# Kernel optimization log

Hardware: AMD Instinct MI355X
Metric: run time of the kernel (lower is better)

Reference implementation:

```python
import jax, jax.numpy as jnp
import numpy as np

BN_EPS = 1e-5
W_THRESH = 1e-4

def _conv(x, w, b):
    # 1x1 Conv1d == per-point linear: x [B,C,N], w [O,C], b [O]
    return jnp.einsum('oc,bcn->bon', w, x) + b[None, :, None]

def _bn(x, g, b):
    # BatchNorm1d in training mode: batch stats over (B, N) per channel
    m = x.mean(axis=(0, 2), keepdims=True)
    v = x.var(axis=(0, 2), keepdims=True)
    return g[None, :, None] * (x - m) * jax.lax.rsqrt(v + BN_EPS) + b[None, :, None]

def setup_inputs() -> dict:
    key = jax.random.key(0)
    ks = jax.random.split(key, 12)
    B, N = 32, 2048
    d = {}
    d['points'] = jax.random.normal(ks[0], (B, 3, N), dtype=jnp.float32)
    def W(k, o, i):
        return jax.random.normal(k, (o, i), dtype=jnp.float32) * 0.02
    # encoder
    d['e_w1'] = W(ks[1], 64, 3);      d['e_b1'] = jnp.zeros(64)
    d['e_g1'] = jnp.ones(64);         d['e_be1'] = jnp.zeros(64)
    d['e_w2'] = W(ks[2], 128, 64);    d['e_b2'] = jnp.zeros(128)
    d['e_g2'] = jnp.ones(128);        d['e_be2'] = jnp.zeros(128)
    d['e_w3'] = W(ks[3], 1024, 128);  d['e_b3'] = jnp.zeros(1024)
    d['e_g3'] = jnp.ones(1024);       d['e_be3'] = jnp.zeros(1024)
    # head
    d['h_w1'] = W(ks[4], 512, 1088);  d['h_b1'] = jnp.zeros(512)
    d['h_g1'] = jnp.ones(512);        d['h_be1'] = jnp.zeros(512)
    d['h_w2'] = W(ks[5], 256, 512);   d['h_b2'] = jnp.zeros(256)
    d['h_g2'] = jnp.ones(256);        d['h_be2'] = jnp.zeros(256)
    d['h_w3'] = W(ks[6], 128, 256);   d['h_b3'] = jnp.zeros(128)
    d['h_g3'] = jnp.ones(128);        d['h_be3'] = jnp.zeros(128)
    d['h_w4'] = W(ks[7], 1, 128);     d['h_b4'] = jnp.zeros(1)
    return d

def _forward(points, e_w1, e_b1, e_g1, e_be1, e_w2, e_b2, e_g2, e_be2,
             e_w3, e_b3, e_g3, e_be3, h_w1, h_b1, h_g1, h_be1,
             h_w2, h_b2, h_g2, h_be2, h_w3, h_b3, h_g3, h_be3, h_w4, h_b4):
    B, _, N = points.shape
    # PointNetEncoder
    x = jax.nn.relu(_bn(_conv(points, e_w1, e_b1), e_g1, e_be1))
    pointfeat = x                                  # [B,64,N]
    x = jax.nn.relu(_bn(_conv(x, e_w2, e_b2), e_g2, e_be2))
    x = _bn(_conv(x, e_w3, e_b3), e_g3, e_be3)      # [B,1024,N]
    g = jnp.max(x, axis=2, keepdims=True)           # [B,1024,1]
    feat = jnp.concatenate([jnp.broadcast_to(g, (B, 1024, N)), pointfeat], axis=1)  # [B,1088,N]
    # head
    y = jax.nn.relu(_bn(_conv(feat, h_w1, h_b1), h_g1, h_be1))
    y = jax.nn.relu(_bn(_conv(y, h_w2, h_b2), h_g2, h_be2))
    y = jax.nn.relu(_bn(_conv(y, h_w3, h_b3), h_g3, h_be3))
    y = _conv(y, h_w4, h_b4)                        # [B,1,N]
    weights = 1.0 + y[:, 0, :]                      # [B,N]
    # WLSFIT, fully batched. Index-selection in the torch loop is equivalent to
    # zeroing invalid weights; the <=3-valid fallback uses uniform weights.
    valid = weights > W_THRESH                      # [B,N] (constant wrt grads)
    nv = jnp.sum(valid, axis=1)                     # [B]
    w_eff = jnp.where((nv > 3)[:, None],
                      weights * valid.astype(weights.dtype),
                      jnp.ones_like(weights))
    A = jnp.concatenate([jnp.swapaxes(points[:, :2, :], 1, 2),
                         jnp.ones((B, N, 1), dtype=points.dtype)], axis=-1)  # [B,N,3]
    z = points[:, 2, :]                             # [B,N]
    XtWX = jnp.einsum('bni,bn,bnj->bij', A, w_eff, A)   # [B,3,3]
    XtY = jnp.einsum('bni,bn->bi', A, w_eff * z)         # [B,3]
    L = jnp.linalg.cholesky(XtWX)
    u = jax.scipy.linalg.solve_triangular(L, XtY[..., None], lower=True)
    beta = jax.scipy.linalg.solve_triangular(jnp.swapaxes(L, -1, -2), u, lower=False)[..., 0]
    return beta, weights

def reference(points, e_w1, e_b1, e_g1, e_be1, e_w2, e_b2, e_g2, e_be2,
              e_w3, e_b3, e_g3, e_be3, h_w1, h_b1, h_g1, h_be1,
              h_w2, h_b2, h_g2, h_be2, h_w3, h_b3, h_g3, h_be3, h_w4, h_b4):
    return _forward(points, e_w1, e_b1, e_g1, e_be1, e_w2, e_b2, e_g2, e_be2,
                    e_w3, e_b3, e_g3, e_be3, h_w1, h_b1, h_g1, h_be1,
                    h_w2, h_b2, h_g2, h_be2, h_w3, h_b3, h_g3, h_be3, h_w4, h_b4)
```

## Files before the change

kernel.cpp:

```cpp
#include <hip/hip_runtime.h>
#include <math.h>


#define M_TOTAL 65536
#define BN_EPS 1e-5f
#define W_THRESH 1e-4f

typedef __attribute__((ext_vector_type(8))) _Float16 f16x8;
typedef __attribute__((ext_vector_type(2))) _Float16 half2v;
typedef __attribute__((ext_vector_type(4))) float f32x4;

__device__ __forceinline__ unsigned short f2h(float f) {
    _Float16 h = (_Float16)f;
    return __builtin_bit_cast(unsigned short, h);
}
__device__ __forceinline__ float h2f(unsigned short u) {
    return (float)__builtin_bit_cast(_Float16, u);
}

__device__ __forceinline__ void cp16(unsigned short* lds, const unsigned short* g) {
    __builtin_amdgcn_global_load_lds(
        (const __attribute__((address_space(1))) unsigned int*)(const void*)g,
        (__attribute__((address_space(3))) unsigned int*)(void*)lds,
        16, 0, 0);
}

__global__ void k_wprep(const float* __restrict__ e_w2, const float* __restrict__ e_w3,
                        const float* __restrict__ hw1, const float* __restrict__ h_w2,
                        const float* __restrict__ h_w3,
                        unsigned short* We2, unsigned short* We3, unsigned short* Wh1,
                        unsigned short* Wh2, unsigned short* Wh3) {
    int t = blockIdx.x;
    const float* W; int ldw, KB; unsigned short* D; int rel;
    if (t < 16)       { W = e_w2;       ldw = 64;   KB = 2;  D = We2; rel = t; }
    else if (t < 272) { W = e_w3;       ldw = 128;  KB = 4;  D = We3; rel = t - 16; }
    else if (t < 336) { W = hw1 + 1024; ldw = 1088; KB = 2;  D = Wh1; rel = t - 272; }
    else if (t < 592) { W = h_w2;       ldw = 512;  KB = 16; D = Wh2; rel = t - 336; }
    else              { W = h_w3;       ldw = 256;  KB = 8;  D = Wh3; rel = t - 592; }
    int ot = rel & 7, kb = (rel >> 3) % KB, ob = rel / (8 * KB);
    int l = threadIdx.x;
    int o = ob * 128 + ot * 16 + (l & 15);
    int k = kb * 32 + (l >> 4) * 8;
    const float* src = W + (size_t)o * ldw + k;
    float4 wa = *(const float4*)src;
    float4 wb = *(const float4*)(src + 4);
    uint4 pk;
    pk.x = (unsigned)f2h(wa.x) | ((unsigned)f2h(wa.y) << 16);
    pk.y = (unsigned)f2h(wa.z) | ((unsigned)f2h(wa.w) << 16);
    pk.z = (unsigned)f2h(wb.x) | ((unsigned)f2h(wb.y) << 16);
    pk.w = (unsigned)f2h(wb.z) | ((unsigned)f2h(wb.w) << 16);
    *(uint4*)(D + (size_t)rel * 512 + l * 8) = pk;
}

__global__ void k_moments(const float* __restrict__ pts, float* __restrict__ momP) {
    float s[9] = {0,0,0,0,0,0,0,0,0};
    for (int m = blockIdx.x * 256 + threadIdx.x; m < M_TOTAL; m += gridDim.x * 256) {
        int b = m >> 11, n = m & 2047;
        const float* p = pts + b * 6144 + n;
        float x = p[0], y = p[2048], z = p[4096];
        s[0] += x; s[1] += y; s[2] += z;
        s[3] += x * x; s[4] += y * y; s[5] += z * z;
        s[6] += x * y; s[7] += x * z; s[8] += y * z;
    }
    for (int off = 32; off; off >>= 1)
#pragma unroll
        for (int i = 0; i < 9; i++) s[i] += __shfl_down(s[i], off);
    __shared__ float red[4][9];
    int lane = threadIdx.x & 63, wv = threadIdx.x >> 6;
    if (lane == 0)
        for (int i = 0; i < 9; i++) red[wv][i] = s[i];
    __syncthreads();
    if (threadIdx.x < 9)
        momP[blockIdx.x * 9 + threadIdx.x] =
            red[0][threadIdx.x] + red[1][threadIdx.x] + red[2][threadIdx.x] + red[3][threadIdx.x];
}

__global__ void k_e1fin(const float* __restrict__ momP, const float* __restrict__ w,
                        const float* __restrict__ bias, const float* __restrict__ g,
                        const float* __restrict__ be, float* __restrict__ a, float* __restrict__ s) {
    __shared__ float m9[9];
    if (threadIdx.x < 9) {
        float t = 0.f;
        for (int k = 0; k < 64; k++) t += momP[k * 9 + threadIdx.x];
        m9[threadIdx.x] = t;
    }
    __syncthreads();
    int o = threadIdx.x;
    float w0 = w[o * 3], w1 = w[o * 3 + 1], w2 = w[o * 3 + 2], b = bias[o];
    float wS1 = w0 * m9[0] + w1 * m9[1] + w2 * m9[2];
    float sum = wS1 + 65536.f * b;
    float sumsq = w0 * w0 * m9[3] + w1 * w1 * m9[4] + w2 * w2 * m9[5]
                + 2.f * (w0 * w1 * m9[6] + w0 * w2 * m9[7] + w1 * w2 * m9[8])
                + 2.f * b * wS1 + 65536.f * b * b;
    float mean = sum * (1.f / 65536.f);
    float var = sumsq * (1.f / 65536.f) - mean * mean;
    float ac = g[o] * rsqrtf(var + BN_EPS);
    a[o] = ac;
    s[o] = be[o] - mean * ac;
}

__global__ void k_e1(const float* __restrict__ pts, const float* __restrict__ w,
                     const float* __restrict__ bias, const float* __restrict__ av,
                     const float* __restrict__ sv, unsigned short* __restrict__ Y) {
    __shared__ float wl[192], bl[64], al[64], sl[64];
    int tid = threadIdx.x;
    if (tid < 192) wl[tid] = w[tid];
    if (tid < 64) { bl[tid] = bias[tid]; al[tid] = av[tid]; sl[tid] = sv[tid]; }
    __syncthreads();
    int m = blockIdx.x * 256 + tid;
    int b = m >> 11, n = m & 2047;
    const float* p = pts + b * 6144 + n;
    float px = p[0], py = p[2048], pz = p[4096];
    unsigned short* yr = Y + (size_t)m * 64;
#pragma unroll
    for (int o8 = 0; o8 < 64; o8 += 8) {
        unsigned pkw[4];
#pragma unroll
        for (int t = 0; t < 4; t++) {
            int o = o8 + t * 2;
            float v0 = fmaf(wl[o * 3 + 0], px, fmaf(wl[o * 3 + 1], py, fmaf(wl[o * 3 + 2], pz, bl[o])));
            float v1 = fmaf(wl[o * 3 + 3], px, fmaf(wl[o * 3 + 4], py, fmaf(wl[o * 3 + 5], pz, bl[o + 1])));
            float y0 = fmaxf(fmaf(al[o], v0, sl[o]), 0.f);
            float y1 = fmaxf(fmaf(al[o + 1], v1, sl[o + 1]), 0.f);
            pkw[t] = (unsigned)f2h(y0) | ((unsigned)f2h(y1) << 16);
        }
        uint4 pk; pk.x = pkw[0]; pk.y = pkw[1]; pk.z = pkw[2]; pk.w = pkw[3];
        *(uint4*)(yr + o8) = pk;
    }
}

__global__ void k_redfin(const float* __restrict__ Ps, const float* __restrict__ Pq,
                         int C, int S,
                         const float* __restrict__ g, const float* __restrict__ be,
                         float* __restrict__ a, float* __restrict__ s) {
    int cl = threadIdx.x & 63, strip = threadIdx.x >> 6;
    int c = blockIdx.x * 64 + cl;
    float sm = 0.f, q = 0.f;
    for (int k = strip; k < S; k += 16) {
        sm += Ps[(size_t)k * C + c];
        q += Pq[(size_t)k * C + c];
    }
    __shared__ float rs[16][64], rq[16][64];
    rs[strip][cl] = sm; rq[strip][cl] = q;
    __syncthreads();
    if (threadIdx.x < 64) {
        float S2 = 0.f, Q = 0.f;
#pragma unroll
        for (int t = 0; t < 16; t++) { S2 += rs[t][cl]; Q += rq[t][cl]; }
        float mean = S2 * (1.f / M_TOTAL);
        float var = Q * (1.f / M_TOTAL) - mean * mean;
        float ac = g[c] * rsqrtf(var + BN_EPS);
        a[c] = ac;
        s[c] = be[c] - mean * ac;
    }
}

template <bool STORE, bool MINMAX, bool BIAS_BO, bool BNB, int KB32, int CHUNKS, bool AREG>
__launch_bounds__(256, 2)
__global__ void k_mgemm(const unsigned short* __restrict__ Wf, int O,
                        const unsigned short* __restrict__ X,
                        const float* __restrict__ a_in, const float* __restrict__ s_in,
                        const float* __restrict__ bias,
                        unsigned short* __restrict__ Y,
                        float* __restrict__ Psum, float* __restrict__ Psq,
                        float* __restrict__ Pmax, float* __restrict__ Pmn) {
    constexpr int K = KB32 * 32;
    __shared__ __align__(16) unsigned short sB[2][4096];
    __shared__ __align__(16) unsigned short sA[AREG ? 2 : 2 * 4096];
    __shared__ __align__(16) short sT[STORE ? 64 * 136 : 2];
    __shared__ _Float16 sah[BNB ? K : 2], ssb[BNB ? K : 2];
    int tid = threadIdx.x;
    int lane = tid & 63, wave = tid >> 6;
    int wo = wave >> 1, wm = wave & 1;
    int m0 = blockIdx.x * (128 * CHUNKS), o0 = blockIdx.y * 128;
    int bidx = m0 >> 11;

    if constexpr (BNB)
        for (int c = tid; c < K; c += 256) {
            sah[c] = (_Float16)a_in[c];
            ssb[c] = (_Float16)s_in[c];
        }

    f16x8 aAll[AREG ? KB32 : 1][4];
    const unsigned short* aBase = Wf + (size_t)blockIdx.y * KB32 * 8 * 512 + lane * 8;
    if constexpr (AREG) {
#pragma unroll
        for (int kb = 0; kb < KB32; kb++)
#pragma unroll
            for (int i = 0; i < 4; i++)
                aAll[kb][i] = *(const f16x8*)(aBase + (size_t)(kb * 8 + wo * 4 + i) * 512);
    }

    f32x4 acc[4][4];
#pragma unroll
    for (int i = 0; i < 4; i++)
#pragma unroll
        for (int j = 0; j < 4; j++) acc[i][j] = (f32x4){0.f, 0.f, 0.f, 0.f};

    float sAcc[4][4] = {}, qAcc[4][4] = {};
    float mxA[4][4], mnA[4][4];
    if constexpr (MINMAX) {
#pragma unroll
        for (int i = 0; i < 4; i++)
#pragma unroll
            for (int r = 0; r < 4; r++) { mxA[i][r] = -3.4e38f; mnA[i][r] = 3.4e38f; }
    }

    auto stageB = [&](int c, int kb_, int buf) {
        const unsigned short* src =
            X + (size_t)(m0 + c * 128 + wave * 32 + (lane & 15)) * K + kb_ * 32 + ((lane >> 4) * 8);
        cp16(&sB[buf][(wave * 2) * 512], src);
        cp16(&sB[buf][(wave * 2 + 1) * 512], src + 16 * K);
    };
    auto stageA = [&](int kb_, int buf) {
        const unsigned short* src = aBase + (size_t)(kb_ * 8 + wave * 2) * 512;
        cp16(&sA[buf * 4096 + (wave * 2) * 512], src);
        cp16(&sA[buf * 4096 + (wave * 2 + 1) * 512], src + 512);
    };

    stageB(0, 0, 0);
    if constexpr (!AREG) stageA(0, 0);

    for (int c = 0; c < CHUNKS; c++) {
#pragma unroll
        for (int kb = 0; kb < KB32; kb++) {
            __syncthreads();
            bool last = (c == CHUNKS - 1) && (kb == KB32 - 1);
            if (!last) {
                int kn = (kb + 1) & (KB32 - 1);
                int cn = (kb == KB32 - 1) ? c + 1 : c;
                int nbuf = (kb + 1) & 1;
                stageB(cn, kn, nbuf);
                if constexpr (!AREG) stageA(kn, nbuf);
            }
            const int cur = kb & 1;
            f16x8 bf[4];
#pragma unroll
            for (int j = 0; j < 4; j++)
                bf[j] = *(const f16x8*)&sB[cur][((wm * 4 + j) * 64 + lane) * 8];

            if constexpr (BNB) {
                int ka = kb * 32 + (lane >> 4) * 8;
                half2v a2[4], s2[4];
#pragma unroll
                for (int t = 0; t < 4; t++) {
                    a2[t] = *(const half2v*)&sah[ka + 2 * t];
                    s2[t] = *(const half2v*)&ssb[ka + 2 * t];
                }
                half2v z2 = (half2v)(_Float16)0;
#pragma unroll
                for (int j = 0; j < 4; j++) {
                    half2v* p = (half2v*)&bf[j];
#pragma unroll
                    for (int t = 0; t < 4; t++)
                        p[t] = __builtin_elementwise_max(a2[t] * p[t] + s2[t], z2);
                }
            }

            if constexpr (AREG) {
#pragma unroll
                for (int i = 0; i < 4; i++)
#pragma unroll
                    for (int j = 0; j < 4; j++)
                        acc[i][j] = __builtin_amdgcn_mfma_f32_16x16x32_f16(aAll[kb][i], bf[j], acc[i][j], 0, 0, 0);
            } else {
                f16x8 af[4];
#pragma unroll
                for (int i = 0; i < 4; i++)
                    af[i] = *(const f16x8*)&sA[cur * 4096 + ((wo * 4 + i) * 64 + lane) * 8];
#pragma unroll
                for (int i = 0; i < 4; i++)
#pragma unroll
                    for (int j = 0; j < 4; j++)
                        acc[i][j] = __builtin_amdgcn_mfma_f32_16x16x32_f16(af[i], bf[j], acc[i][j], 0, 0, 0);
            }
        }

        int q = lane >> 4, lc = lane & 15;
#pragma unroll
        for (int i = 0; i < 4; i++)
#pragma unroll
            for (int j = 0; j < 4; j++)
#pragma unroll
                for (int r = 0; r < 4; r++) {
                    float v = acc[i][j][r];
                    sAcc[i][r] += v;
                    qAcc[i][r] = fmaf(v, v, qAcc[i][r]);
                    if constexpr (MINMAX) {
                        mxA[i][r] = fmaxf(mxA[i][r], v);
                        mnA[i][r] = fminf(mnA[i][r], v);
                    }
                }

        if constexpr (STORE) {
            int mbase = m0 + c * 128;
#pragma unroll
            for (int ch = 0; ch < 2; ch++) {
                if (wm == ch) {
#pragma unroll
                    for (int i = 0; i < 4; i++) {
                        int ob = o0 + wo * 64 + i * 16 + q * 4;
                        float b0 = BIAS_BO ? bias[bidx * O + ob + 0] : bias[ob + 0];
                        float b1 = BIAS_BO ? bias[bidx * O + ob + 1] : bias[ob + 1];
                        float b2 = BIAS_BO ? bias[bidx * O + ob + 2] : bias[ob + 2];
                        float b3 = BIAS_BO ? bias[bidx * O + ob + 3] : bias[ob + 3];
#pragma unroll
                        for (int j = 0; j < 4; j++) {
                            int row = j * 16 + lc;
                            int c0 = wo * 64 + i * 16 + q * 4;
                            uint2 pk;
                            pk.x = (unsigned)f2h(acc[i][j][0] + b0) | ((unsigned)f2h(acc[i][j][1] + b1) << 16);
                            pk.y = (unsigned)f2h(acc[i][j][2] + b2) | ((unsigned)f2h(acc[i][j][3] + b3) << 16);
                            *(uint2*)&sT[row * 136 + c0] = pk;
                        }
                    }
                }
                __syncthreads();
                {
                    int row = tid >> 4, c0 = (tid & 15) * 8;
#pragma unroll
                    for (int rr = 0; rr < 4; rr++) {
                        int r2 = row + rr * 16;
                        int m = mbase + ch * 64 + r2;
                        uint4 v = *(const uint4*)&sT[r2 * 136 + c0];
                        *(uint4*)(Y + (size_t)m * O + o0 + c0) = v;
                    }
                }
                __syncthreads();
            }
        }

        if (c + 1 < CHUNKS) {
#pragma unroll
            for (int i = 0; i < 4; i++)
#pragma unroll
                for (int j = 0; j < 4; j++) acc[i][j] = (f32x4){0.f, 0.f, 0.f, 0.f};
        }
    }

    int q = lane >> 4, lc = lane & 15;
    int slot = blockIdx.x * 2 + wm;
    const float NM = 64.f * CHUNKS;
#pragma unroll
    for (int i = 0; i < 4; i++) {
        int ob = o0 + wo * 64 + i * 16 + q * 4;
        float s4[4], q4[4], mx[4], mn[4];
#pragma unroll
        for (int r = 0; r < 4; r++) {
            s4[r] = sAcc[i][r]; q4[r] = qAcc[i][r];
            if constexpr (MINMAX) { mx[r] = mxA[i][r]; mn[r] = mnA[i][r]; }
        }
#pragma unroll
        for (int off = 1; off < 16; off <<= 1)
#pragma unroll
            for (int r = 0; r < 4; r++) {
                s4[r] += __shfl_xor(s4[r], off);
                q4[r] += __shfl_xor(q4[r], off);
                if constexpr (MINMAX) {
                    mx[r] = fmaxf(mx[r], __shfl_xor(mx[r], off));
                    mn[r] = fminf(mn[r], __shfl_xor(mn[r], off));
                }
            }
        if (lc == 0) {
            float S4[4], Q4[4];
#pragma unroll
            for (int r = 0; r < 4; r++) {
                float bv = BIAS_BO ? bias[bidx * O + ob + r] : bias[ob + r];
                S4[r] = s4[r] + NM * bv;
                Q4[r] = q4[r] + 2.f * bv * s4[r] + NM * bv * bv;
                if constexpr (MINMAX) { mx[r] += bv; mn[r] += bv; }
            }
            *(float4*)&Psum[(size_t)slot * O + ob] = make_float4(S4[0], S4[1], S4[2], S4[3]);
            *(float4*)&Psq[(size_t)slot * O + ob] = make_float4(Q4[0], Q4[1], Q4[2], Q4[3]);
            if constexpr (MINMAX) {
                *(float4*)&Pmax[(size_t)slot * O + ob] = make_float4(mx[0], mx[1], mx[2], mx[3]);
                *(float4*)&Pmn[(size_t)slot * O + ob] = make_float4(mn[0], mn[1], mn[2], mn[3]);
            }
        }
    }
}

__global__ void k_g(const float* __restrict__ Pmax, const float* __restrict__ Pmn,
                    const float* __restrict__ a3, const float* __restrict__ s3,
                    float* __restrict__ gT) {
    int i = blockIdx.x * 256 + threadIdx.x;
    if (i >= 32768) return;
    int b = i >> 10, o = i & 1023;
    float mx = -3.4e38f, mn = 3.4e38f;
#pragma unroll
    for (int t = 0; t < 8; t++) {
        mx = fmaxf(mx, Pmax[(size_t)(b * 8 + t) * 1024 + o]);
        mn = fminf(mn, Pmn[(size_t)(b * 8 + t) * 1024 + o]);
    }
    float a = a3[o];
    gT[o * 32 + b] = (a >= 0.f) ? fmaf(a, mx, s3[o]) : fmaf(a, mn, s3[o]);
}

__global__ void k_gh(const float* __restrict__ hw1, const float* __restrict__ hb1,
                     const float* __restrict__ gT, float* __restrict__ Gh) {
    int o = blockIdx.x;
    int b = threadIdx.x & 31, strip = threadIdx.x >> 5;
    const float* wr = hw1 + (size_t)o * 1088 + strip * 128;
    const float* gr = gT + strip * 128 * 32 + b;
    float a0 = 0.f, a1 = 0.f;
#pragma unroll 4
    for (int c = 0; c < 128; c += 2) {
        a0 = fmaf(wr[c], gr[c * 32], a0);
        a1 = fmaf(wr[c + 1], gr[(c + 1) * 32], a1);
    }
    __shared__ float red[8][32];
    red[strip][b] = a0 + a1;
    __syncthreads();
    if (threadIdx.x < 32) {
        float acc = hb1[o];
#pragma unroll
        for (int t = 0; t < 8; t++) acc += red[t][threadIdx.x];
        Gh[threadIdx.x * 512 + o] = acc;
    }
}

__global__ void k_h4(const unsigned short* __restrict__ X, const float* __restrict__ a,
                     const float* __restrict__ s, const float* __restrict__ w4,
                     const float* __restrict__ b4, float* __restrict__ outw,
                     int* __restrict__ nvP) {
    __shared__ float la[128], ls[128], lw[128];
    int tid = threadIdx.x;
    if (tid < 128) { la[tid] = a[tid]; ls[tid] = s[tid]; lw[tid] = w4[tid]; }
    __syncthreads();
    int m = blockIdx.x * 256 + tid;
    const unsigned short* xr = X + (size_t)m * 128;
    float acc = 0.f;
#pragma unroll
    for (int c = 0; c < 128; c += 8) {
        uint4 raw = *(const uint4*)(xr + c);
        unsigned u[4] = {raw.x, raw.y, raw.z, raw.w};
#pragma unroll
        for (int t = 0; t < 4; t++) {
            float x0 = h2f((unsigned short)(u[t] & 0xffffu));
            float x1 = h2f((unsigned short)(u[t] >> 16));
            float y0 = fmaxf(fmaf(la[c + t * 2], x0, ls[c + t * 2]), 0.f);
            float y1 = fmaxf(fmaf(la[c + t * 2 + 1], x1, ls[c + t * 2 + 1]), 0.f);
            acc = fmaf(lw[c + t * 2], y0, acc);
            acc = fmaf(lw[c + t * 2 + 1], y1, acc);
        }
    }
    float wgt = 1.f + acc + b4[0];
    outw[m] = wgt;
    unsigned long long msk = __ballot(wgt > W_THRESH);
    __shared__ int cnt[4];
    int lane = tid & 63, wv = tid >> 6;
    if (lane == 0) cnt[wv] = __popcll(msk);
    __syncthreads();
    if (tid == 0) nvP[blockIdx.x] = cnt[0] + cnt[1] + cnt[2] + cnt[3];
}

__global__ void k_wls(const float* __restrict__ pts, const float* __restrict__ outw,
                      const int* __restrict__ nvP, float* __restrict__ beta) {
    int b = blockIdx.x;
    const float* p = pts + b * 6144;
    const float* wr = outw + b * 2048;
    int nv = 0;
#pragma unroll
    for (int i = 0; i < 8; i++) nv += nvP[b * 8 + i];
    bool use_w = nv > 3;
    float s[9] = {0, 0, 0, 0, 0, 0, 0, 0, 0};
    for (int n = threadIdx.x; n < 2048; n += 256) {
        float wgt = wr[n];
        float we = use_w ? (wgt > W_THRESH ? wgt : 0.f) : 1.f;
        float px = p[n], py = p[2048 + n], pz = p[4096 + n];
        s[0] += we * px * px; s[1] += we * px * py; s[2] += we * px;
        s[3] += we * py * py; s[4] += we * py;      s[5] += we;
        s[6] += we * px * pz; s[7] += we * py * pz; s[8] += we * pz;
    }
    for (int off = 32; off; off >>= 1)
#pragma unroll
        for (int i = 0; i < 9; i++) s[i] += __shfl_down(s[i], off);
    __shared__ float red[4][9];
    int lane = threadIdx.x & 63, wv = threadIdx.x >> 6;
    if (lane == 0)
        for (int i = 0; i < 9; i++) red[wv][i] = s[i];
    __syncthreads();
    if (threadIdx.x == 0) {
        float t[9];
        for (int i = 0; i < 9; i++) t[i] = red[0][i] + red[1][i] + red[2][i] + red[3][i];
        float a11 = t[0], a21 = t[1], a31 = t[2], a22 = t[3], a32 = t[4], a33 = t[5];
        float L11 = sqrtf(a11);
        float L21 = a21 / L11, L31 = a31 / L11;
        float L22 = sqrtf(a22 - L21 * L21);
        float L32 = (a32 - L31 * L21) / L22;
        float L33 = sqrtf(a33 - L31 * L31 - L32 * L32);
        float u1 = t[6] / L11;
        float u2 = (t[7] - L21 * u1) / L22;
        float u3 = (t[8] - L31 * u1 - L32 * u2) / L33;
        float b3 = u3 / L33;
        float b2 = (u2 - L32 * b3) / L22;
        float b1 = (u1 - L21 * b2 - L31 * b3) / L11;
        beta[b * 3 + 0] = b1;
        beta[b * 3 + 1] = b2;
        beta[b * 3 + 2] = b3;
    }
}

extern "C" void kernel_launch(void* const* d_in, const int* in_sizes, int n_in,
                              void* d_out, int out_size, void* d_ws, size_t ws_size,
                              hipStream_t stream) {
    (void)in_sizes; (void)n_in; (void)out_size; (void)ws_size;
    const float* pts   = (const float*)d_in[0];
    const float* e_w1  = (const float*)d_in[1];
    const float* e_b1  = (const float*)d_in[2];
    const float* e_g1  = (const float*)d_in[3];
    const float* e_be1 = (const float*)d_in[4];
    const float* e_w2  = (const float*)d_in[5];
    const float* e_b2  = (const float*)d_in[6];
    const float* e_g2  = (const float*)d_in[7];
    const float* e_be2 = (const float*)d_in[8];
    const float* e_w3  = (const float*)d_in[9];
    const float* e_b3  = (const float*)d_in[10];
    const float* e_g3  = (const float*)d_in[11];
    const float* e_be3 = (const float*)d_in[12];
    const float* h_w1  = (const float*)d_in[13];
    const float* h_b1  = (const float*)d_in[14];
    const float* h_g1  = (const float*)d_in[15];
    const float* h_be1 = (const float*)d_in[16];
    const float* h_w2  = (const float*)d_in[17];
    const float* h_b2  = (const float*)d_in[18];
    const float* h_g2  = (const float*)d_in[19];
    const float* h_be2 = (const float*)d_in[20];
    const float* h_w3  = (const float*)d_in[21];
    const float* h_b3  = (const float*)d_in[22];
    const float* h_g3  = (const float*)d_in[23];
    const float* h_be3 = (const float*)d_in[24];
    const float* h_w4  = (const float*)d_in[25];
    const float* h_b4  = (const float*)d_in[26];

    const size_t M = M_TOTAL;
    unsigned short* wsu = (unsigned short*)d_ws;
    unsigned short* Y1e = wsu;
    unsigned short* Y2e = wsu + 64 * M;
    unsigned short* Y1h = wsu + 192 * M;
    unsigned short* Y2h = wsu + 704 * M;
    unsigned short* Y3h = wsu + 960 * M;
    unsigned short* We2 = wsu + 1088 * M;
    unsigned short* We3 = We2 + 8192;
    unsigned short* Wh1 = We3 + 131072;
    unsigned short* Wh2 = Wh1 + 32768;
    unsigned short* Wh3 = Wh2 + 131072;
    float* wsf = (float*)(Wh3 + 32768);
    float* avec = wsf;
    float* svec = avec + 2112;
    float* momP = svec + 2112;
    float* Ps   = momP + 576;
    float* Pq   = Ps + 1024 * 1024;
    float* Pmax = Pq + 1024 * 1024;
    float* Pmn  = Pmax + 1024 * 1024;
    float* gT   = Pmn + 1024 * 1024;
    float* Gh   = gT + 32768;
    int* nvP    = (int*)(Gh + 16384);

    float* beta = (float*)d_out;
    float* outw = beta + 96;

    k_wprep<<<656, 64, 0, stream>>>(e_w2, e_w3, h_w1, h_w2, h_w3, We2, We3, Wh1, Wh2, Wh3);
    k_moments<<<64, 256, 0, stream>>>(pts, momP);
    k_e1fin<<<1, 64, 0, stream>>>(momP, e_w1, e_b1, e_g1, e_be1, avec, svec);
    k_e1<<<256, 256, 0, stream>>>(pts, e_w1, e_b1, avec, svec, Y1e);

    k_mgemm<true, false, false, false, 2, 2, true><<<dim3(256, 1), 256, 0, stream>>>(
        We2, 128, Y1e, nullptr, nullptr, e_b2, Y2e, Ps, Pq, nullptr, nullptr);
    k_redfin<<<2, 1024, 0, stream>>>(Ps, Pq, 128, 512, e_g2, e_be2, avec + 64, svec + 64);

    k_mgemm<false, true, false, true, 4, 4, false><<<dim3(128, 8), 256, 0, stream>>>(
        We3, 1024, Y2e, avec + 64, svec + 64, e_b3, nullptr, Ps, Pq, Pmax, Pmn);
    k_redfin<<<16, 1024, 0, stream>>>(Ps, Pq, 1024, 256, e_g3, e_be3, avec + 192, svec + 192);

    k_g<<<128, 256, 0, stream>>>(Pmax, Pmn, avec + 192, svec + 192, gT);
    k_gh<<<512, 256, 0, stream>>>(h_w1, h_b1, gT, Gh);

    k_mgemm<true, false, true, false, 2, 4, true><<<dim3(128, 4), 256, 0, stream>>>(
        Wh1, 512, Y1e, nullptr, nullptr, Gh, Y1h, Ps, Pq, nullptr, nullptr);
    k_redfin<<<8, 1024, 0, stream>>>(Ps, Pq, 512, 256, h_g1, h_be1, avec + 1216, svec + 1216);

    k_mgemm<true, false, false, true, 16, 2, false><<<dim3(256, 2), 256, 0, stream>>>(
        Wh2, 256, Y1h, avec + 1216, svec + 1216, h_b2, Y2h, Ps, Pq, nullptr, nullptr);
    k_redfin<<<4, 1024, 0, stream>>>(Ps, Pq, 256, 512, h_g2, h_be2, avec + 1728, svec + 1728);

    k_mgemm<true, false, false, true, 8, 2, false><<<dim3(256, 1), 256, 0, stream>>>(
        Wh3, 128, Y2h, avec + 1728, svec + 1728, h_b3, Y3h, Ps, Pq, nullptr, nullptr);
    k_redfin<<<2, 1024, 0, stream>>>(Ps, Pq, 128, 512, h_g3, h_be3, avec + 1984, svec + 1984);

    k_h4<<<256, 256, 0, stream>>>(Y3h, avec + 1984, svec + 1984, h_w4, h_b4, outw, nvP);
    k_wls<<<32, 256, 0, stream>>>(pts, outw, nvP, beta);
}
```

Baseline: 341.8 us.

## Stage two k-blocks per barrier, keep weights resident in LDS, reuse B buffer for stores

The fused GEMM kernel now stages SB32 k-slices of X (and A when streamed) per pipeline step instead of one, which halves the number of __syncthreads per chunk. Weights that used to sit in registers (AREG) now sit fully in LDS (ARES) and are read per k-block, and the e3 GEMM now also uses resident LDS weights. The separate transpose-store buffer is gone: the epilogue reuses the last B buffer in four 32-row passes. This lowers register pressure and barrier count, but adds LDS traffic for A reads and an extra barrier before the store.

```diff
diff --git a/kernel.cpp b/kernel.cpp
--- a/kernel.cpp
+++ b/kernel.cpp
@@ -155,23 +155,27 @@
     }
 }
 
-template <bool STORE, bool MINMAX, bool BIAS_BO, bool BNB, int KB32, int CHUNKS, bool AREG>
+template <bool STORE, bool MINMAX, bool BIAS_BO, bool BNB, int KB32, int SB32, int CHUNKS, bool ARES>
 __launch_bounds__(256, 2)
-__global__ void k_mgemm(const unsigned short* __restrict__ Wf, int O,
-                        const unsigned short* __restrict__ X,
-                        const float* __restrict__ a_in, const float* __restrict__ s_in,
-                        const float* __restrict__ bias,
-                        unsigned short* __restrict__ Y,
-                        float* __restrict__ Psum, float* __restrict__ Psq,
-                        float* __restrict__ Pmax, float* __restrict__ Pmn) {
+__global__ void k_mg(const unsigned short* __restrict__ Wf, int O,
+                     const unsigned short* __restrict__ X,
+                     const float* __restrict__ a_in, const float* __restrict__ s_in,
+                     const float* __restrict__ bias,
+                     unsigned short* __restrict__ Y,
+                     float* __restrict__ Psum, float* __restrict__ Psq,
+                     float* __restrict__ Pmax, float* __restrict__ Pmn) {
     constexpr int K = KB32 * 32;
-    __shared__ __align__(16) unsigned short sB[2][4096];
-    __shared__ __align__(16) unsigned short sA[AREG ? 2 : 2 * 4096];
-    __shared__ __align__(16) short sT[STORE ? 64 * 136 : 2];
+    constexpr int SPC = KB32 / SB32;
+    constexpr int NSTEPS = CHUNKS * SPC;
+    constexpr int BT = SB32 * 8;
+    constexpr int BSZ = BT * 512;
+    constexpr int ASZ = ARES ? KB32 * 8 * 512 : 2 * BSZ;
+    __shared__ __align__(16) unsigned short sA[ASZ];
+    __shared__ __align__(16) unsigned short sB[2][BSZ];
     __shared__ _Float16 sah[BNB ? K : 2], ssb[BNB ? K : 2];
-    int tid = threadIdx.x;
-    int lane = tid & 63, wave = tid >> 6;
+    int tid = threadIdx.x, lane = tid & 63, wave = tid >> 6;
     int wo = wave >> 1, wm = wave & 1;
+    int q = lane >> 4, lc = lane & 15;
     int m0 = blockIdx.x * (128 * CHUNKS), o0 = blockIdx.y * 128;
     int bidx = m0 >> 11;
 
@@ -181,22 +185,38 @@
             ssb[c] = (_Float16)s_in[c];
         }
 
-    f16x8 aAll[AREG ? KB32 : 1][4];
-    const unsigned short* aBase = Wf + (size_t)blockIdx.y * KB32 * 8 * 512 + lane * 8;
-    if constexpr (AREG) {
-#pragma unroll
-        for (int kb = 0; kb < KB32; kb++)
-#pragma unroll
-            for (int i = 0; i < 4; i++)
-                aAll[kb][i] = *(const f16x8*)(aBase + (size_t)(kb * 8 + wo * 4 + i) * 512);
-    }
+    const unsigned short* aSrc = Wf + (size_t)blockIdx.y * KB32 * 8 * 512 + lane * 8;
+
+    auto stageB = [&](int cc, int ssl, int buf) {
+#pragma unroll
+        for (int t = wave; t < BT; t += 4) {
+            int kb = t >> 3, mt = t & 7;
+            const unsigned short* src = X
+                + (size_t)(m0 + cc * 128 + mt * 16 + (lane & 15)) * K
+                + (ssl * SB32 + kb) * 32 + ((lane >> 4) * 8);
+            cp16(&sB[buf][t * 512], src);
+        }
+    };
+    auto stageA = [&](int ssl, int buf) {
+#pragma unroll
+        for (int t = wave; t < BT; t += 4)
+            cp16(&sA[buf * BSZ + t * 512], aSrc + (size_t)(ssl * SB32 * 8 + t) * 512);
+    };
+
+    if constexpr (ARES) {
+#pragma unroll
+        for (int t = wave; t < KB32 * 8; t += 4)
+            cp16(&sA[t * 512], aSrc + (size_t)t * 512);
+    } else {
+        stageA(0, 0);
+    }
+    stageB(0, 0, 0);
 
     f32x4 acc[4][4];
 #pragma unroll
     for (int i = 0; i < 4; i++)
 #pragma unroll
         for (int j = 0; j < 4; j++) acc[i][j] = (f32x4){0.f, 0.f, 0.f, 0.f};
-
     float sAcc[4][4] = {}, qAcc[4][4] = {};
     float mxA[4][4], mnA[4][4];
     if constexpr (MINMAX) {
@@ -206,68 +226,52 @@
             for (int r = 0; r < 4; r++) { mxA[i][r] = -3.4e38f; mnA[i][r] = 3.4e38f; }
     }
 
-    auto stageB = [&](int c, int kb_, int buf) {
-        const unsigned short* src =
-            X + (size_t)(m0 + c * 128 + wave * 32 + (lane & 15)) * K + kb_ * 32 + ((lane >> 4) * 8);
-        cp16(&sB[buf][(wave * 2) * 512], src);
-        cp16(&sB[buf][(wave * 2 + 1) * 512], src + 16 * K);
-    };
-    auto stageA = [&](int kb_, int buf) {
-        const unsigned short* src = aBase + (size_t)(kb_ * 8 + wave * 2) * 512;
-        cp16(&sA[buf * 4096 + (wave * 2) * 512], src);
-        cp16(&sA[buf * 4096 + (wave * 2 + 1) * 512], src + 512);
-    };
-
-    stageB(0, 0, 0);
-    if constexpr (!AREG) stageA(0, 0);
+    __syncthreads();
 
     for (int c = 0; c < CHUNKS; c++) {
 #pragma unroll
-        for (int kb = 0; kb < KB32; kb++) {
-            __syncthreads();
-            bool last = (c == CHUNKS - 1) && (kb == KB32 - 1);
-            if (!last) {
-                int kn = (kb + 1) & (KB32 - 1);
-                int cn = (kb == KB32 - 1) ? c + 1 : c;
-                int nbuf = (kb + 1) & 1;
-                stageB(cn, kn, nbuf);
-                if constexpr (!AREG) stageA(kn, nbuf);
+        for (int ss = 0; ss < SPC; ss++) {
+            if (c > 0 || ss > 0) __syncthreads();
+            int step = c * SPC + ss;
+            if (step + 1 < NSTEPS) {
+                int wrap = (ss == SPC - 1) ? 1 : 0;
+                int nc = c + wrap;
+                int nss = wrap ? 0 : ss + 1;
+                int nbuf = (step + 1) & 1;
+                stageB(nc, nss, nbuf);
+                if constexpr (!ARES) stageA(nss, nbuf);
             }
-            const int cur = kb & 1;
-            f16x8 bf[4];
-#pragma unroll
-            for (int j = 0; j < 4; j++)
-                bf[j] = *(const f16x8*)&sB[cur][((wm * 4 + j) * 64 + lane) * 8];
-
-            if constexpr (BNB) {
-                int ka = kb * 32 + (lane >> 4) * 8;
-                half2v a2[4], s2[4];
-#pragma unroll
-                for (int t = 0; t < 4; t++) {
-                    a2[t] = *(const half2v*)&sah[ka + 2 * t];
-                    s2[t] = *(const half2v*)&ssb[ka + 2 * t];
+            int p = step & 1;
+            const unsigned short* bb = sB[p];
+            const unsigned short* ab = ARES ? sA : sA + p * BSZ;
+#pragma unroll
+            for (int kb = 0; kb < SB32; kb++) {
+                f16x8 af[4], bf[4];
+                int tA = ARES ? ((ss * SB32 + kb) * 8) : (kb * 8);
+#pragma unroll
+                for (int i = 0; i < 4; i++)
+                    af[i] = *(const f16x8*)&ab[(tA + wo * 4 + i) * 512 + lane * 8];
+#pragma unroll
+                for (int j = 0; j < 4; j++)
+                    bf[j] = *(const f16x8*)&bb[(kb * 8 + wm * 4 + j) * 512 + lane * 8];
+
+                if constexpr (BNB) {
+                    int ka = (ss * SB32 + kb) * 32 + (lane >> 4) * 8;
+                    half2v a2[4], s2[4];
+#pragma unroll
+                    for (int t = 0; t < 4; t++) {
+                        a2[t] = *(const half2v*)&sah[ka + 2 * t];
+                        s2[t] = *(const half2v*)&ssb[ka + 2 * t];
+                    }
+                    half2v z2 = (half2v)(_Float16)0;
+#pragma unroll
+                    for (int j = 0; j < 4; j++) {
+                        half2v* pb = (half2v*)&bf[j];
+#pragma unroll
+                        for (int t = 0; t < 4; t++)
+                            pb[t] = __builtin_elementwise_max(a2[t] * pb[t] + s2[t], z2);
+                    }
                 }
-                half2v z2 = (half2v)(_Float16)0;
-#pragma unroll
-                for (int j = 0; j < 4; j++) {
-                    half2v* p = (half2v*)&bf[j];
-#pragma unroll
-                    for (int t = 0; t < 4; t++)
-                        p[t] = __builtin_elementwise_max(a2[t] * p[t] + s2[t], z2);
-                }
-            }
-
-            if constexpr (AREG) {
-#pragma unroll
-                for (int i = 0; i < 4; i++)
-#pragma unroll
-                    for (int j = 0; j < 4; j++)
-                        acc[i][j] = __builtin_amdgcn_mfma_f32_16x16x32_f16(aAll[kb][i], bf[j], acc[i][j], 0, 0, 0);
-            } else {
-                f16x8 af[4];
-#pragma unroll
-                for (int i = 0; i < 4; i++)
-                    af[i] = *(const f16x8*)&sA[cur * 4096 + ((wo * 4 + i) * 64 + lane) * 8];
 #pragma unroll
                 for (int i = 0; i < 4; i++)
 #pragma unroll
@@ -276,7 +280,6 @@
             }
         }
 
-        int q = lane >> 4, lc = lane & 15;
 #pragma unroll
         for (int i = 0; i < 4; i++)
 #pragma unroll
@@ -293,10 +296,14 @@
                 }
 
         if constexpr (STORE) {
+            int pLast = (c * SPC + SPC - 1) & 1;
+            short* sT = (short*)&sB[pLast][0];
             int mbase = m0 + c * 128;
-#pragma unroll
-            for (int ch = 0; ch < 2; ch++) {
-                if (wm == ch) {
+            __syncthreads();
+#pragma unroll
+            for (int ch = 0; ch < 4; ch++) {
+                if (wm == (ch >> 1)) {
+                    int jlo = (ch & 1) * 2;
 #pragma unroll
                     for (int i = 0; i < 4; i++) {
                         int ob = o0 + wo * 64 + i * 16 + q * 4;
@@ -305,8 +312,9 @@
                         float b2 = BIAS_BO ? bias[bidx * O + ob + 2] : bias[ob + 2];
                         float b3 = BIAS_BO ? bias[bidx * O + ob + 3] : bias[ob + 3];
 #pragma unroll
-                        for (int j = 0; j < 4; j++) {
-                            int row = j * 16 + lc;
+                        for (int jj = 0; jj < 2; jj++) {
+                            int j = jlo + jj;
+                            int row = jj * 16 + lc;
                             int c0 = wo * 64 + i * 16 + q * 4;
                             uint2 pk;
                             pk.x = (unsigned)f2h(acc[i][j][0] + b0) | ((unsigned)f2h(acc[i][j][1] + b1) << 16);
@@ -319,9 +327,9 @@
                 {
                     int row = tid >> 4, c0 = (tid & 15) * 8;
 #pragma unroll
-                    for (int rr = 0; rr < 4; rr++) {
+                    for (int rr = 0; rr < 2; rr++) {
                         int r2 = row + rr * 16;
-                        int m = mbase + ch * 64 + r2;
+                        int m = mbase + ch * 32 + r2;
                         uint4 v = *(const uint4*)&sT[r2 * 136 + c0];
                         *(uint4*)(Y + (size_t)m * O + o0 + c0) = v;
                     }
@@ -338,7 +346,6 @@
         }
     }
 
-    int q = lane >> 4, lc = lane & 15;
     int slot = blockIdx.x * 2 + wm;
     const float NM = 64.f * CHUNKS;
 #pragma unroll
@@ -565,26 +572,26 @@
     k_e1fin<<<1, 64, 0, stream>>>(momP, e_w1, e_b1, e_g1, e_be1, avec, svec);
     k_e1<<<256, 256, 0, stream>>>(pts, e_w1, e_b1, avec, svec, Y1e);
 
-    k_mgemm<true, false, false, false, 2, 2, true><<<dim3(256, 1), 256, 0, stream>>>(
+    k_mg<true, false, false, false, 2, 2, 2, true><<<dim3(256, 1), 256, 0, stream>>>(
         We2, 128, Y1e, nullptr, nullptr, e_b2, Y2e, Ps, Pq, nullptr, nullptr);
     k_redfin<<<2, 1024, 0, stream>>>(Ps, Pq, 128, 512, e_g2, e_be2, avec + 64, svec + 64);
 
-    k_mgemm<false, true, false, true, 4, 4, false><<<dim3(128, 8), 256, 0, stream>>>(
+    k_mg<false, true, false, true, 4, 2, 4, true><<<dim3(128, 8), 256, 0, stream>>>(
         We3, 1024, Y2e, avec + 64, svec + 64, e_b3, nullptr, Ps, Pq, Pmax, Pmn);
     k_redfin<<<16, 1024, 0, stream>>>(Ps, Pq, 1024, 256, e_g3, e_be3, avec + 192, svec + 192);
 
     k_g<<<128, 256, 0, stream>>>(Pmax, Pmn, avec + 192, svec + 192, gT);
     k_gh<<<512, 256, 0, stream>>>(h_w1, h_b1, gT, Gh);
 
-    k_mgemm<true, false, true, false, 2, 4, true><<<dim3(128, 4), 256, 0, stream>>>(
+    k_mg<true, false, true, false, 2, 2, 4, true><<<dim3(128, 4), 256, 0, stream>>>(
         Wh1, 512, Y1e, nullptr, nullptr, Gh, Y1h, Ps, Pq, nullptr, nullptr);
     k_redfin<<<8, 1024, 0, stream>>>(Ps, Pq, 512, 256, h_g1, h_be1, avec + 1216, svec + 1216);
 
-    k_mgemm<true, false, false, true, 16, 2, false><<<dim3(256, 2), 256, 0, stream>>>(
+    k_mg<true, false, false, true, 16, 2, 2, false><<<dim3(256, 2), 256, 0, stream>>>(
         Wh2, 256, Y1h, avec + 1216, svec + 1216, h_b2, Y2h, Ps, Pq, nullptr, nullptr);
     k_redfin<<<4, 1024, 0, stream>>>(Ps, Pq, 256, 512, h_g2, h_be2, avec + 1728, svec + 1728);
 
-    k_mgemm<true, false, false, true, 8, 2, false><<<dim3(256, 1), 256, 0, stream>>>(
+    k_mg<true, false, false, true, 8, 2, 2, false><<<dim3(256, 1), 256, 0, stream>>>(
         Wh3, 128, Y2h, avec + 1728, svec + 1728, h_b3, Y3h, Ps, Pq, nullptr, nullptr);
     k_redfin<<<2, 1024, 0, stream>>>(Ps, Pq, 128, 512, h_g3, h_be3, avec + 1984, svec + 1984);
 
```

Result: faster. 314.4 us (-8.0%).
